# Optimization experiments

Measured on AMD Instinct MI355X. Metric: run time of the kernel, lower is better.

The kernel has to match this reference:

```python
import jax, jax.numpy as jnp
import numpy as np

H, DQS, DQP, DVS, DVP = 12, 16, 4, 16, 8
S_SCALAR = (3.0 * DQS) ** -0.5
S_POINT = (3.0 * DQP * (9.0 * 2.0 ** 0.5)) ** -0.5
S_PAIR = 3.0 ** -0.5
_OFF = np.cumsum([0, H * DQS, H * DQS, H * DVS, H * DQP * 3, H * DQP * 3, H * DVP * 3])


def _ln(x, g, b, eps=1e-5):
    mu = x.mean(-1, keepdims=True)
    var = x.var(-1, keepdims=True)
    return (x - mu) / jnp.sqrt(var + eps) * g + b


def setup_inputs() -> dict:
    B, N, D, PD = 2, 512, 384, 128
    key = jax.random.key(0)
    ks = jax.random.split(key, 12)
    node_feats = jax.random.normal(ks[0], (B, N, D), jnp.float32)
    pair_feats = jax.random.normal(ks[1], (B, N, N, PD), jnp.float32)
    mask = jnp.ones((B, N), dtype=bool)
    # random per-residue rigid frames (orthonormal rotations via QR)
    rot = jnp.linalg.qr(jax.random.normal(ks[2], (B, N, 3, 3), jnp.float32))[0]
    trans = jax.random.normal(ks[3], (B, N, 3), jnp.float32)
    dim_qkv = int(_OFF[-1])             # 1152
    dim_out = H * (PD + DVS + 4 * DVP)  # 2112
    s = 0.02
    p = dict(
        ln_s_g=jnp.ones((D,)), ln_s_b=jnp.zeros((D,)),
        ln_p_g=jnp.ones((PD,)), ln_p_b=jnp.zeros((PD,)),
        w_pair_bias=s * jax.random.normal(ks[4], (PD, H), jnp.float32),
        w_qkv=s * jax.random.normal(ks[5], (D, dim_qkv), jnp.float32),
        point_weights=jnp.full((1, H, 1, 1), float(np.log(np.e - 1.0)), jnp.float32),
        w_out=s * jax.random.normal(ks[6], (dim_out, D), jnp.float32),
        b_out=jnp.zeros((D,)),
        ln_t_g=jnp.ones((D,)), ln_t_b=jnp.zeros((D,)),
        w_ff1=s * jax.random.normal(ks[7], (D, 4 * D), jnp.float32),
        b_ff1=jnp.zeros((4 * D,)),
        w_ff2=s * jax.random.normal(ks[8], (4 * D, D), jnp.float32),
        b_ff2=jnp.zeros((D,)),
    )
    return dict(node_feats=node_feats, pair_feats=pair_feats, mask=mask,
                rot=rot, trans=trans, **p)


def reference(node_feats, pair_feats, mask, rot, trans,
              ln_s_g, ln_s_b, ln_p_g, ln_p_b, w_pair_bias, w_qkv,
              point_weights, w_out, b_out,
              ln_t_g, ln_t_b, w_ff1, b_ff1, w_ff2, b_ff2):
    b, n, d = node_feats.shape
    x = _ln(node_feats, ln_s_g, ln_s_b)
    p = _ln(pair_feats, ln_p_g, ln_p_b)
    pair_bias = jnp.einsum('bijd,dh->bhij', p, w_pair_bias)
    qkv = x @ w_qkv  # (b,n,1152)

    def heads(t, dh):
        return t.reshape(b, n, H, dh).transpose(0, 2, 1, 3)  # b h n d

    q_s = heads(qkv[..., _OFF[0]:_OFF[1]], DQS)
    k_s = heads(qkv[..., _OFF[1]:_OFF[2]], DQS)
    v_s = heads(qkv[..., _OFF[2]:_OFF[3]], DVS)

    def to_pts(t, dp):
        pts = t.reshape(b, n, H * dp, 3)
        # rigid apply: R_i @ x + t_i (global frame)
        pts = jnp.einsum('bnxy,bnpy->bnpx', rot, pts) + trans[:, :, None, :]
        return pts.reshape(b, n, H, dp, 3).transpose(0, 2, 1, 3, 4)  # b h n d 3

    q_p = to_pts(qkv[..., _OFF[3]:_OFF[4]], DQP)
    k_p = to_pts(qkv[..., _OFF[4]:_OFF[5]], DQP)
    v_p = to_pts(qkv[..., _OFF[5]:_OFF[6]], DVP)

    scalar_logits = jnp.einsum('bhid,bhjd->bhij', q_s, k_s)
    # dist attn: -sum_{d,c} (q-k)^2, expanded to avoid (b,h,n,n,d,3) intermediate
    qq = jnp.sum(q_p * q_p, axis=(-1, -2))
    kk = jnp.sum(k_p * k_p, axis=(-1, -2))
    qk = jnp.einsum('bhidc,bhjdc->bhij', q_p, k_p)
    point_logits = -(qq[..., :, None] + kk[..., None, :] - 2.0 * qk)
    point_logits = point_logits * jax.nn.softplus(point_weights)

    neg = jnp.finfo(node_feats.dtype).min
    pm = mask[:, None, :, None] & mask[:, None, None, :]  # b 1 i j
    scalar_logits = jnp.where(pm, scalar_logits, neg)
    point_logits = jnp.where(pm, point_logits, neg)
    pair_bias = jnp.where(pm, pair_bias, neg)

    logits = S_SCALAR * scalar_logits + S_POINT * point_logits + S_PAIR * pair_bias
    attn = jax.nn.softmax(logits, axis=-1)

    out_s = jnp.einsum('bhij,bhjd->bhid', attn, v_s)
    out_pair = jnp.einsum('bhij,bijd->bhid', attn, p)
    out_p = jnp.einsum('bhij,bhjdc->bhidc', attn, v_p)
    # rigid inverse: R_i^T (x - t_i) back to local frame
    pts = out_p.transpose(0, 2, 1, 3, 4).reshape(b, n, H * DVP, 3)
    pts = jnp.einsum('bnyx,bnpy->bnpx', rot, pts - trans[:, :, None, :])
    out_p = pts.reshape(b, n, H, DVP, 3)
    pnorm = jnp.sqrt(jnp.sum(out_p * out_p, axis=-1) + 1e-8)  # safe_norm

    cat = jnp.concatenate([
        out_s.transpose(0, 2, 1, 3).reshape(b, n, H * DVS),
        out_p.reshape(b, n, H * DVP * 3),
        pnorm.reshape(b, n, H * DVP),
        out_pair.transpose(0, 2, 1, 3).reshape(b, n, -1),
    ], axis=-1)
    attn_out = cat @ w_out + b_out

    # residuals + transition (dropout=0 -> identity). Note: transition is
    # applied to attn_out (pre-residual), exactly as in the torch forward.
    node1 = attn_out + node_feats
    t = _ln(attn_out, ln_t_g, ln_t_b)
    t = jax.nn.gelu(t @ w_ff1 + b_ff1) @ w_ff2 + b_ff2
    return t + node1
```

## Files before the change

kernel.cpp:

```cpp
#include <hip/hip_runtime.h>
#include <hip/hip_bf16.h>
#include <math.h>

typedef __hip_bfloat16 bf16;
typedef _Float16 f16;
typedef unsigned short ushort_t;
typedef ushort_t ushort8 __attribute__((ext_vector_type(8)));
typedef ushort_t us4 __attribute__((ext_vector_type(4)));
typedef short bf16x8 __attribute__((ext_vector_type(8)));
typedef f16 f16x8 __attribute__((ext_vector_type(8)));
typedef f16 f16x2 __attribute__((ext_vector_type(2)));
typedef float f32x4 __attribute__((ext_vector_type(4)));
typedef unsigned int u32x4 __attribute__((ext_vector_type(4)));

constexpr float S_SCALAR = 0.14433756729740643f;
constexpr float S_POINT  = 0.08091531528f;
constexpr float S_PAIR   = 0.5773502691896258f;

__device__ inline short f2bfs(float x) {
  return (short)__builtin_bit_cast(unsigned short, __float2bfloat16(x));
}
__device__ inline ushort_t f2bfu(float x) {
  return (ushort_t)__builtin_bit_cast(unsigned short, __float2bfloat16(x));
}
__device__ inline ushort_t f2hu(float x) {
  return __builtin_bit_cast(ushort_t, (f16)x);
}
__device__ inline float h2f(ushort_t u) {
  return (float)__builtin_bit_cast(f16, u);
}
__device__ inline float fdot2f(unsigned a, unsigned b, float c) {
#if __has_builtin(__builtin_amdgcn_fdot2)
  return __builtin_amdgcn_fdot2(__builtin_bit_cast(f16x2, a),
                                __builtin_bit_cast(f16x2, b), c, false);
#else
  f16x2 av = __builtin_bit_cast(f16x2, a), bv = __builtin_bit_cast(f16x2, b);
  return c + (float)av[0] * (float)bv[0] + (float)av[1] * (float)bv[1];
#endif
}

__device__ inline float gelu_tanh(float x) {
  float c = 0.7978845608028654f * (x + 0.044715f * x * x * x);
  return 0.5f * x * (1.f + tanhf(c));
}

__global__ __launch_bounds__(128) void ln384_kernel(
    const float* __restrict__ in, const float* __restrict__ g,
    const float* __restrict__ b, float* __restrict__ out)
{
  int row = blockIdx.x;
  const float* x = in + (size_t)row * 384;
  int t = threadIdx.x;
  float v[3]; float s = 0.f, s2 = 0.f;
#pragma unroll
  for (int i = 0; i < 3; i++) { v[i] = x[t + 128 * i]; s += v[i]; s2 += v[i] * v[i]; }
  for (int o = 32; o; o >>= 1) { s += __shfl_down(s, o); s2 += __shfl_down(s2, o); }
  __shared__ float sh[4];
  int wid = t >> 6, lane = t & 63;
  if (lane == 0) { sh[wid] = s; sh[2 + wid] = s2; }
  __syncthreads();
  s = sh[0] + sh[1]; s2 = sh[2] + sh[3];
  float mean = s * (1.f / 384.f);
  float var = s2 * (1.f / 384.f) - mean * mean;
  float rstd = rsqrtf(fmaxf(var, 0.f) + 1e-5f);
  float* orow = out + (size_t)row * 384;
#pragma unroll
  for (int i = 0; i < 3; i++) {
    int c = t + 128 * i;
    orow[c] = (v[i] - mean) * rstd * g[c] + b[c];
  }
}

__global__ __launch_bounds__(256) void prep_all_kernel(
    const float* __restrict__ w_qkv, const float* __restrict__ w_out,
    const float* __restrict__ w_ff1, const float* __restrict__ w_ff2,
    ushort_t* __restrict__ wqkvT, ushort_t* __restrict__ woutT,
    ushort_t* __restrict__ wff1T, ushort_t* __restrict__ wff2T,
    const float* __restrict__ g, const float* __restrict__ bb,
    const float* __restrict__ wpb, ushort_t* __restrict__ gwbT,
    float* __restrict__ gsbs,
    const float* __restrict__ node, const float* __restrict__ ln_s_g,
    const float* __restrict__ ln_s_b, float* __restrict__ xout)
{
  __shared__ float shmem[2048];
  int bid = blockIdx.x;
  int t = threadIdx.x;
  if (bid < 2376) {
    const float* src; ushort_t* dst; int K, N, bx, by;
    if (bid < 432)       { src = w_qkv; dst = wqkvT; K = 384;  N = 1152; bx = bid % 36;          by = bid / 36; }
    else if (bid < 1224) { src = w_out; dst = woutT; K = 2112; N = 384;  bx = (bid - 432) % 12;  by = (bid - 432) / 12; }
    else if (bid < 1800) { src = w_ff1; dst = wff1T; K = 384;  N = 1536; bx = (bid - 1224) % 48; by = (bid - 1224) / 48; }
    else                 { src = w_ff2; dst = wff2T; K = 1536; N = 384;  bx = (bid - 1800) % 12; by = (bid - 1800) / 12; }
    float (&tile)[32][33] = *reinterpret_cast<float (*)[32][33]>(shmem);
    int n0 = bx * 32, k0 = by * 32;
    int c = t & 31, r4 = (t >> 5) * 4;
#pragma unroll
    for (int i = 0; i < 4; i++)
      tile[r4 + i][c] = src[(size_t)(k0 + r4 + i) * N + n0 + c];
    __syncthreads();
#pragma unroll
    for (int i = 0; i < 4; i++)
      dst[(size_t)(n0 + r4 + i) * K + k0 + c] = f2bfu(tile[c][r4 + i]);
    return;
  }
  if (bid == 2376) {
    for (int idx = t; idx < 2048; idx += 256) {
      int h = idx >> 7, c = idx & 127;
      float v = (h < 12) ? g[c] * wpb[c * 12 + h] : 0.f;
      bf16 r = __float2bfloat16(v);
      gwbT[idx] = __builtin_bit_cast(unsigned short, r);
      shmem[idx] = __bfloat162float(r);
    }
    __syncthreads();
    if (t < 16) {
      float s = 0.f;
      for (int c = 0; c < 128; c++) s += shmem[t * 128 + c];
      gsbs[t] = s;
    } else if (t < 32) {
      int h = t - 16;
      float s = 0.f;
      if (h < 12) for (int c = 0; c < 128; c++) s = fmaf(bb[c], wpb[c * 12 + h], s);
      gsbs[t] = s;
    }
    return;
  }
  int half = t >> 7, tt = t & 127;
  int row = (bid - 2377) * 2 + half;
  const float* x = node + (size_t)row * 384;
  float v[3]; float s = 0.f, s2 = 0.f;
#pragma unroll
  for (int i = 0; i < 3; i++) { v[i] = x[tt + 128 * i]; s += v[i]; s2 += v[i] * v[i]; }
  for (int o = 32; o; o >>= 1) { s += __shfl_down(s, o); s2 += __shfl_down(s2, o); }
  int wid = t >> 6, lane = t & 63;
  if (lane == 0) { shmem[wid] = s; shmem[4 + wid] = s2; }
  __syncthreads();
  s = shmem[half * 2] + shmem[half * 2 + 1];
  s2 = shmem[4 + half * 2] + shmem[4 + half * 2 + 1];
  float mean = s * (1.f / 384.f);
  float var = s2 * (1.f / 384.f) - mean * mean;
  float rstd = rsqrtf(fmaxf(var, 0.f) + 1e-5f);
  float* orow = xout + (size_t)row * 384;
#pragma unroll
  for (int i = 0; i < 3; i++) {
    int c = tt + 128 * i;
    orow[c] = (v[i] - mean) * rstd * ln_s_g[c] + ln_s_b[c];
  }
}

template <int EPI>
__global__ __launch_bounds__(256) void gemm_mfma_kernel(
    const float* __restrict__ A, const ushort_t* __restrict__ BT,
    const float* __restrict__ bias, const float* __restrict__ r1,
    const float* __restrict__ r2, float* __restrict__ C,
    int M, int Nn, int K)
{
  __shared__ ushort_t As[64][72];
  __shared__ ushort_t Bs[64][72];
  int t = threadIdx.x;
  int w = t >> 6, l = t & 63;
  int m0 = blockIdx.y * 64, n0 = blockIdx.x * 64;
  int wm = (w >> 1) * 32, wn = (w & 1) * 32;
  int lr = l & 15, lk = l >> 4;
  int sr = t >> 2, sc = (t & 3) * 16;
  f32x4 acc[2][2];
#pragma unroll
  for (int i = 0; i < 2; i++)
#pragma unroll
    for (int j = 0; j < 2; j++) acc[i][j] = (f32x4){0.f, 0.f, 0.f, 0.f};

  for (int k0 = 0; k0 < K; k0 += 64) {
    const float* Ar = A + (size_t)(m0 + sr) * K + k0 + sc;
    const ushort_t* Br = BT + (size_t)(n0 + sr) * K + k0 + sc;
    float4 a0 = *(const float4*)(Ar + 0);
    float4 a1 = *(const float4*)(Ar + 4);
    float4 a2 = *(const float4*)(Ar + 8);
    float4 a3 = *(const float4*)(Ar + 12);
    ushort8 b0 = *(const ushort8*)(Br + 0);
    ushort8 b1 = *(const ushort8*)(Br + 8);
    ushort8 u0, u1;
    u0[0] = f2bfu(a0.x); u0[1] = f2bfu(a0.y); u0[2] = f2bfu(a0.z); u0[3] = f2bfu(a0.w);
    u0[4] = f2bfu(a1.x); u0[5] = f2bfu(a1.y); u0[6] = f2bfu(a1.z); u0[7] = f2bfu(a1.w);
    u1[0] = f2bfu(a2.x); u1[1] = f2bfu(a2.y); u1[2] = f2bfu(a2.z); u1[3] = f2bfu(a2.w);
    u1[4] = f2bfu(a3.x); u1[5] = f2bfu(a3.y); u1[6] = f2bfu(a3.z); u1[7] = f2bfu(a3.w);
    *(ushort8*)&As[sr][sc] = u0;
    *(ushort8*)&As[sr][sc + 8] = u1;
    *(ushort8*)&Bs[sr][sc] = b0;
    *(ushort8*)&Bs[sr][sc + 8] = b1;
    __syncthreads();
#pragma unroll
    for (int kk = 0; kk < 2; kk++) {
      bf16x8 af0 = *(const bf16x8*)&As[wm + lr][kk * 32 + lk * 8];
      bf16x8 af1 = *(const bf16x8*)&As[wm + 16 + lr][kk * 32 + lk * 8];
      bf16x8 bf0 = *(const bf16x8*)&Bs[wn + lr][kk * 32 + lk * 8];
      bf16x8 bf1 = *(const bf16x8*)&Bs[wn + 16 + lr][kk * 32 + lk * 8];
      acc[0][0] = __builtin_amdgcn_mfma_f32_16x16x32_bf16(af0, bf0, acc[0][0], 0, 0, 0);
      acc[0][1] = __builtin_amdgcn_mfma_f32_16x16x32_bf16(af0, bf1, acc[0][1], 0, 0, 0);
      acc[1][0] = __builtin_amdgcn_mfma_f32_16x16x32_bf16(af1, bf0, acc[1][0], 0, 0, 0);
      acc[1][1] = __builtin_amdgcn_mfma_f32_16x16x32_bf16(af1, bf1, acc[1][1], 0, 0, 0);
    }
    __syncthreads();
  }
#pragma unroll
  for (int mf = 0; mf < 2; mf++) {
#pragma unroll
    for (int nf = 0; nf < 2; nf++) {
      int nn = n0 + wn + nf * 16 + lr;
      float bv = bias ? bias[nn] : 0.f;
#pragma unroll
      for (int e = 0; e < 4; e++) {
        int m = m0 + wm + mf * 16 + lk * 4 + e;
        float v = acc[mf][nf][e] + bv;
        if (EPI == 1) v = gelu_tanh(v);
        if (EPI == 2) v += r1[(size_t)m * Nn + nn] + r2[(size_t)m * Nn + nn];
        C[(size_t)m * Nn + nn] = v;
      }
    }
  }
}

template <int EPI>
__global__ __launch_bounds__(256) void gemm_mfma_m32_kernel(
    const float* __restrict__ A, const ushort_t* __restrict__ BT,
    const float* __restrict__ bias, const float* __restrict__ r1,
    const float* __restrict__ r2, float* __restrict__ C,
    int M, int Nn, int K)
{
  __shared__ ushort_t As[32][72];
  __shared__ ushort_t Bs[64][72];
  int t = threadIdx.x;
  int w = t >> 6, l = t & 63;
  int m0 = blockIdx.y * 32, n0 = blockIdx.x * 64;
  int wm = (w & 1) * 16, wn = (w >> 1) * 32;
  int lr = l & 15, lk = l >> 4;
  int ar = t >> 3, ac = (t & 7) * 8;
  int br = t >> 2, bc = (t & 3) * 16;
  f32x4 acc[2];
  acc[0] = (f32x4){0.f, 0.f, 0.f, 0.f};
  acc[1] = (f32x4){0.f, 0.f, 0.f, 0.f};

  for (int k0 = 0; k0 < K; k0 += 64) {
    const float* Ar = A + (size_t)(m0 + ar) * K + k0 + ac;
    float4 a0 = *(const float4*)(Ar + 0);
    float4 a1 = *(const float4*)(Ar + 4);
    ushort8 u;
    u[0] = f2bfu(a0.x); u[1] = f2bfu(a0.y); u[2] = f2bfu(a0.z); u[3] = f2bfu(a0.w);
    u[4] = f2bfu(a1.x); u[5] = f2bfu(a1.y); u[6] = f2bfu(a1.z); u[7] = f2bfu(a1.w);
    *(ushort8*)&As[ar][ac] = u;
    const ushort_t* Br = BT + (size_t)(n0 + br) * K + k0 + bc;
    *(ushort8*)&Bs[br][bc] = *(const ushort8*)(Br + 0);
    *(ushort8*)&Bs[br][bc + 8] = *(const ushort8*)(Br + 8);
    __syncthreads();
#pragma unroll
    for (int kk = 0; kk < 2; kk++) {
      bf16x8 af = *(const bf16x8*)&As[wm + lr][kk * 32 + lk * 8];
      bf16x8 bf0 = *(const bf16x8*)&Bs[wn + lr][kk * 32 + lk * 8];
      bf16x8 bf1 = *(const bf16x8*)&Bs[wn + 16 + lr][kk * 32 + lk * 8];
      acc[0] = __builtin_amdgcn_mfma_f32_16x16x32_bf16(af, bf0, acc[0], 0, 0, 0);
      acc[1] = __builtin_amdgcn_mfma_f32_16x16x32_bf16(af, bf1, acc[1], 0, 0, 0);
    }
    __syncthreads();
  }
#pragma unroll
  for (int nf = 0; nf < 2; nf++) {
    int nn = n0 + wn + nf * 16 + lr;
    float bv = bias ? bias[nn] : 0.f;
#pragma unroll
    for (int e = 0; e < 4; e++) {
      int m = m0 + wm + lk * 4 + e;
      float v = acc[nf][e] + bv;
      if (EPI == 1) v = gelu_tanh(v);
      if (EPI == 2) v += r1[(size_t)m * Nn + nn] + r2[(size_t)m * Nn + nn];
      C[(size_t)m * Nn + nn] = v;
    }
  }
}

__global__ __launch_bounds__(256) void qkv_post_kernel(
    const float* __restrict__ qkv, const float* __restrict__ rot,
    const float* __restrict__ trans, const float* __restrict__ pw,
    f16* __restrict__ qhat, f16* __restrict__ khat,
    ushort_t* __restrict__ vT)
{
  int bh = blockIdx.x;
  int b = bh / 12, h = bh - b * 12;
  int role = blockIdx.y >> 1;
  int j = (blockIdx.y & 1) * 256 + threadIdx.x;
  int bn = b * 512 + j;
  const float* row = qkv + (size_t)bn * 1152;
  float R[9];
#pragma unroll
  for (int k = 0; k < 9; k++) R[k] = rot[bn * 9 + k];
  float T0 = trans[bn * 3], T1 = trans[bn * 3 + 1], T2 = trans[bn * 3 + 2];
  if (role == 0) {
    float sp = log1pf(__expf(pw[h]));
    float c1 = 2.f * S_POINT * sp;
    float spp = S_POINT * sp;
    f16* qh = qhat + ((size_t)bh * 512 + j) * 32;
#pragma unroll
    for (int d = 0; d < 16; d++) qh[d] = (f16)(S_SCALAR * row[h * 16 + d]);
#pragma unroll
    for (int p = 0; p < 4; p++) {
      int base = 576 + (h * 4 + p) * 3;
      float x = row[base], y = row[base + 1], z = row[base + 2];
      qh[16 + p * 3 + 0] = (f16)(c1 * (R[0] * x + R[1] * y + R[2] * z + T0));
      qh[16 + p * 3 + 1] = (f16)(c1 * (R[3] * x + R[4] * y + R[5] * z + T1));
      qh[16 + p * 3 + 2] = (f16)(c1 * (R[6] * x + R[7] * y + R[8] * z + T2));
    }
    qh[28] = (f16)(-spp);
    qh[29] = (f16)0.f; qh[30] = (f16)0.f; qh[31] = (f16)0.f;
  } else if (role == 1) {
    f16* kh = khat + ((size_t)bh * 512 + j) * 32;
#pragma unroll
    for (int d = 0; d < 16; d++) kh[d] = (f16)(row[192 + h * 16 + d]);
    float kksum = 0.f;
#pragma unroll
    for (int p = 0; p < 4; p++) {
      int base = 720 + (h * 4 + p) * 3;
      float x = row[base], y = row[base + 1], z = row[base + 2];
      float gx = R[0] * x + R[1] * y + R[2] * z + T0;
      float gy = R[3] * x + R[4] * y + R[5] * z + T1;
      float gz = R[6] * x + R[7] * y + R[8] * z + T2;
      kh[16 + p * 3 + 0] = (f16)gx; kh[16 + p * 3 + 1] = (f16)gy; kh[16 + p * 3 + 2] = (f16)gz;
      kksum = fmaf(gx, gx, kksum); kksum = fmaf(gy, gy, kksum); kksum = fmaf(gz, gz, kksum);
    }
    kh[28] = (f16)kksum;
    kh[29] = (f16)0.f; kh[30] = (f16)0.f; kh[31] = (f16)0.f;
  } else {
    ushort_t* vt = vT + (size_t)bh * 40 * 512;
#pragma unroll
    for (int c = 0; c < 16; c++) vt[c * 512 + j] = f2hu(row[384 + h * 16 + c]);
#pragma unroll
    for (int p = 0; p < 8; p++) {
      int base = 864 + (h * 8 + p) * 3;
      float x = row[base], y = row[base + 1], z = row[base + 2];
      vt[(16 + p * 3 + 0) * 512 + j] = f2hu(R[0] * x + R[1] * y + R[2] * z + T0);
      vt[(16 + p * 3 + 1) * 512 + j] = f2hu(R[3] * x + R[4] * y + R[5] * z + T1);
      vt[(16 + p * 3 + 2) * 512 + j] = f2hu(R[6] * x + R[7] * y + R[8] * z + T2);
    }
  }
}

__global__ __launch_bounds__(256) void mega_kernel(
    const float* __restrict__ pair, const ushort_t* __restrict__ gwbT,
    const float* __restrict__ gsbs, const float* __restrict__ g,
    const float* __restrict__ bb, const f16* __restrict__ qhat,
    const f16* __restrict__ khat, ushort_t* __restrict__ attnb,
    float* __restrict__ cat)
{
  __shared__ ushort_t tile[128][136];
  __shared__ ushort_t Ps[16][520];
  __shared__ ushort_t bias_s[16][136];
  __shared__ unsigned qhat_u[12][16];
  __shared__ float red_s[2][6][4];
  __shared__ float m_s[16], l_s[16], r_s[16], invl_s[16];
  __shared__ float mhist_s[4][16], cf_s[4][16];

  int bn = blockIdx.x;
  int b = bn >> 9, i = bn & 511;
  int t = threadIdx.x;
  int wv = t >> 6, ln = t & 63, lr = ln & 15, lk = ln >> 4;

  if (t < 16) { m_s[t] = -3.0e38f; l_s[t] = 0.f; r_s[t] = 1.f; }
  for (int idx = t; idx < 4 * 520; idx += 256) Ps[12 + idx / 520][idx % 520] = 0;
  if (t < 192) {
    int h = t >> 4, d4 = t & 15;
    qhat_u[h][d4] = ((const unsigned*)qhat)[((size_t)(b * 12 + h) * 512 + i) * 16 + d4];
  }
  bf16x8 bfrag[4];
#pragma unroll
  for (int kc = 0; kc < 4; kc++) {
    const ushort_t* gp = gwbT + lr * 128 + kc * 32 + lk * 8;
    us4 q0 = *(const us4*)gp;
    us4 q1 = *(const us4*)(gp + 4);
    bfrag[kc][0] = (short)q0[0]; bfrag[kc][1] = (short)q0[1];
    bfrag[kc][2] = (short)q0[2]; bfrag[kc][3] = (short)q0[3];
    bfrag[kc][4] = (short)q1[0]; bfrag[kc][5] = (short)q1[1];
    bfrag[kc][6] = (short)q1[2]; bfrag[kc][7] = (short)q1[3];
  }
  float gsum = gsbs[lr];
  float bsP = S_PAIR * gsbs[16 + lr];
  int n0 = wv * 32;
  int sw0 = (((n0 + lr) >> 3) & 7) << 4;
  int sw1 = (((n0 + 16 + lr) >> 3) & 7) << 4;
  f32x4 po0 = {0.f, 0.f, 0.f, 0.f}, po1 = {0.f, 0.f, 0.f, 0.f};
  __syncthreads();

  for (int ck = 0; ck < 4; ck++) {
    int jc = ck * 128;
    const float* p0 = pair + ((size_t)bn * 512 + jc + wv * 32 + lr) * 128 + lk * 8;
    f32x4 acc0 = {0.f, 0.f, 0.f, 0.f}, acc1 = {0.f, 0.f, 0.f, 0.f};
    float s0 = 0.f, s20 = 0.f, s1 = 0.f, s21 = 0.f;
#pragma unroll
    for (int kc = 0; kc < 4; kc++) {
      float4 u0 = *(const float4*)(p0 + kc * 32);
      float4 u1 = *(const float4*)(p0 + kc * 32 + 4);
      float4 w0 = *(const float4*)(p0 + 2048 + kc * 32);
      float4 w1 = *(const float4*)(p0 + 2048 + kc * 32 + 4);
      s0 += u0.x + u0.y + u0.z + u0.w + u1.x + u1.y + u1.z + u1.w;
      s20 = fmaf(u0.x, u0.x, s20); s20 = fmaf(u0.y, u0.y, s20);
      s20 = fmaf(u0.z, u0.z, s20); s20 = fmaf(u0.w, u0.w, s20);
      s20 = fmaf(u1.x, u1.x, s20); s20 = fmaf(u1.y, u1.y, s20);
      s20 = fmaf(u1.z, u1.z, s20); s20 = fmaf(u1.w, u1.w, s20);
      s1 += w0.x + w0.y + w0.z + w0.w + w1.x + w1.y + w1.z + w1.w;
      s21 = fmaf(w0.x, w0.x, s21); s21 = fmaf(w0.y, w0.y, s21);
      s21 = fmaf(w0.z, w0.z, s21); s21 = fmaf(w0.w, w0.w, s21);
      s21 = fmaf(w1.x, w1.x, s21); s21 = fmaf(w1.y, w1.y, s21);
      s21 = fmaf(w1.z, w1.z, s21); s21 = fmaf(w1.w, w1.w, s21);
      bf16x8 a0, a1;
      a0[0] = f2bfs(u0.x); a0[1] = f2bfs(u0.y); a0[2] = f2bfs(u0.z); a0[3] = f2bfs(u0.w);
      a0[4] = f2bfs(u1.x); a0[5] = f2bfs(u1.y); a0[6] = f2bfs(u1.z); a0[7] = f2bfs(u1.w);
      a1[0] = f2bfs(w0.x); a1[1] = f2bfs(w0.y); a1[2] = f2bfs(w0.z); a1[3] = f2bfs(w0.w);
      a1[4] = f2bfs(w1.x); a1[5] = f2bfs(w1.y); a1[6] = f2bfs(w1.z); a1[7] = f2bfs(w1.w);
      acc0 = __builtin_amdgcn_mfma_f32_16x16x32_bf16(a0, bfrag[kc], acc0, 0, 0, 0);
      acc1 = __builtin_amdgcn_mfma_f32_16x16x32_bf16(a1, bfrag[kc], acc1, 0, 0, 0);
    }
    s0 += __shfl_xor(s0, 16);  s0 += __shfl_xor(s0, 32);
    s20 += __shfl_xor(s20, 16); s20 += __shfl_xor(s20, 32);
    s1 += __shfl_xor(s1, 16);  s1 += __shfl_xor(s1, 32);
    s21 += __shfl_xor(s21, 16); s21 += __shfl_xor(s21, 32);
    float mean0 = s0 * (1.f / 128.f);
    float rstd0 = rsqrtf(fmaxf(s20 * (1.f / 128.f) - mean0 * mean0, 0.f) + 1e-5f);
    float mean1 = s1 * (1.f / 128.f);
    float rstd1 = rsqrtf(fmaxf(s21 * (1.f / 128.f) - mean1 * mean1, 0.f) + 1e-5f);
    int jl_u = wv * 32 + lr, jl_w = wv * 32 + 16 + lr;
#pragma unroll
    for (int kc = 0; kc < 4; kc++) {
      int c0 = kc * 32 + lk * 8;
      float4 u0 = *(const float4*)(p0 + kc * 32);
      float4 u1 = *(const float4*)(p0 + kc * 32 + 4);
      float4 w0 = *(const float4*)(p0 + 2048 + kc * 32);
      float4 w1 = *(const float4*)(p0 + 2048 + kc * 32 + 4);
      float4 g0 = *(const float4*)(g + c0);
      float4 g1 = *(const float4*)(g + c0 + 4);
      float4 b0 = *(const float4*)(bb + c0);
      float4 b1 = *(const float4*)(bb + c0 + 4);
      float uu[8] = {u0.x, u0.y, u0.z, u0.w, u1.x, u1.y, u1.z, u1.w};
      float ww[8] = {w0.x, w0.y, w0.z, w0.w, w1.x, w1.y, w1.z, w1.w};
      float gg[8] = {g0.x, g0.y, g0.z, g0.w, g1.x, g1.y, g1.z, g1.w};
      float bv[8] = {b0.x, b0.y, b0.z, b0.w, b1.x, b1.y, b1.z, b1.w};
#pragma unroll
      for (int e = 0; e < 8; e++) {
        int c = c0 + e;
        int sw = ((c >> 3) & 7) << 4;
        tile[c][jl_u ^ sw] = f2hu(fmaf((uu[e] - mean0) * rstd0, gg[e], bv[e]));
        tile[c][jl_w ^ sw] = f2hu(fmaf((ww[e] - mean1) * rstd1, gg[e], bv[e]));
      }
    }
    {
      us4 pk0, pk1;
#pragma unroll
      for (int e = 0; e < 4; e++) {
        int r = lk * 4 + e;
        float m0 = __shfl(mean0, r), rs0 = __shfl(rstd0, r);
        float m1 = __shfl(mean1, r), rs1 = __shfl(rstd1, r);
        pk0[e] = f2hu(fmaf(S_PAIR * rs0, acc0[e] - m0 * gsum, bsP));
        pk1[e] = f2hu(fmaf(S_PAIR * rs1, acc1[e] - m1 * gsum, bsP));
      }
      *(us4*)&bias_s[lr][wv * 32 + lk * 4] = pk0;
      *(us4*)&bias_s[lr][wv * 32 + 16 + lk * 4] = pk1;
    }
    __syncthreads();
    float lgv[6];
#pragma unroll
    for (int q = 0; q < 6; q++) {
      int h = 2 * q + (wv >> 1);
      int jl = (wv & 1) * 64 + ln;
      const u32x4* kr = (const u32x4*)(khat + ((size_t)(b * 12 + h) * 512 + jc + jl) * 32);
      float d = 0.f;
#pragma unroll
      for (int qq = 0; qq < 4; qq++) {
        u32x4 kv = kr[qq];
        u32x4 qv = *(const u32x4*)&qhat_u[h][qq * 4];
        d = fdot2f(kv[0], qv[0], d);
        d = fdot2f(kv[1], qv[1], d);
        d = fdot2f(kv[2], qv[2], d);
        d = fdot2f(kv[3], qv[3], d);
      }
      lgv[q] = d + h2f(bias_s[h][jl]);
    }
#pragma unroll
    for (int q = 0; q < 6; q++) {
      float m = lgv[q];
      m = fmaxf(m, __shfl_xor(m, 1));  m = fmaxf(m, __shfl_xor(m, 2));
      m = fmaxf(m, __shfl_xor(m, 4));  m = fmaxf(m, __shfl_xor(m, 8));
      m = fmaxf(m, __shfl_xor(m, 16)); m = fmaxf(m, __shfl_xor(m, 32));
      if (ln == 0) red_s[0][q][wv] = m;
    }
    __syncthreads();
    if (t < 12) {
      int q = t >> 1, wp = (t & 1) * 2;
      float cm = fmaxf(red_s[0][q][wp], red_s[0][q][wp + 1]);
      float mo = m_s[t];
      float mn = fmaxf(mo, cm);
      m_s[t] = mn; r_s[t] = __expf(mo - mn); mhist_s[ck][t] = mn;
    }
    __syncthreads();
#pragma unroll
    for (int q = 0; q < 6; q++) {
      int h = 2 * q + (wv >> 1);
      int jl = (wv & 1) * 64 + ln;
      float p = __expf(lgv[q] - m_s[h]);
      Ps[h][jc + jl] = f2hu(p);
      float s = p;
      s += __shfl_xor(s, 1);  s += __shfl_xor(s, 2);
      s += __shfl_xor(s, 4);  s += __shfl_xor(s, 8);
      s += __shfl_xor(s, 16); s += __shfl_xor(s, 32);
      if (ln == 0) red_s[1][q][wv] = s;
    }
#pragma unroll
    for (int e = 0; e < 4; e++) {
      float rr = r_s[lk * 4 + e];
      po0[e] *= rr; po1[e] *= rr;
    }
    __syncthreads();
    if (t < 12) {
      int q = t >> 1, wp = (t & 1) * 2;
      l_s[t] = l_s[t] * r_s[t] + red_s[1][q][wp] + red_s[1][q][wp + 1];
    }
#pragma unroll
    for (int ks = 0; ks < 4; ks++) {
      int kb = ks * 32 + lk * 8;
      f16x8 af = *(const f16x8*)&Ps[lr][jc + kb];
      f16x8 b0 = *(const f16x8*)&tile[n0 + lr][kb ^ sw0];
      f16x8 b1 = *(const f16x8*)&tile[n0 + 16 + lr][kb ^ sw1];
      po0 = __builtin_amdgcn_mfma_f32_16x16x32_f16(af, b0, po0, 0, 0, 0);
      po1 = __builtin_amdgcn_mfma_f32_16x16x32_f16(af, b1, po1, 0, 0, 0);
    }
    __syncthreads();
  }
  if (t < 64) {
    int c = t >> 4, h = t & 15;
    cf_s[c][h] = __expf(mhist_s[c][h] - m_s[h]);
  }
  if (t < 16) invl_s[t] = 1.f / l_s[t];
  __syncthreads();
  ushort_t* arow = attnb + (size_t)bn * 12 * 512;
#pragma unroll
  for (int it = 0; it < 24; it++) {
    int idx = t + 256 * it;
    int h = idx >> 9, j = idx & 511;
    float v = h2f(Ps[h][j]) * cf_s[j >> 7][h] * invl_s[h];
    arow[(size_t)h * 512 + j] = f2hu(v);
  }
  float* crow = cat + (size_t)bn * 2112 + 576;
#pragma unroll
  for (int e = 0; e < 4; e++) {
    int hh = lk * 4 + e;
    if (hh < 12) {
      float il = invl_s[hh];
      crow[hh * 128 + n0 + lr] = po0[e] * il;
      crow[hh * 128 + n0 + 16 + lr] = po1[e] * il;
    }
  }
}

__global__ __launch_bounds__(256) void sv_gemm_kernel(
    const ushort_t* __restrict__ attn, const ushort_t* __restrict__ vT,
    float* __restrict__ svraw)
{
  int i0 = blockIdx.x * 64;
  int bh = blockIdx.y;
  int b = bh / 12, h = bh - b * 12;
  __shared__ ushort_t As_[64][72];
  __shared__ ushort_t Bs_[48][72];
  int t = threadIdx.x;
  int w = t >> 6, l = t & 63, lr = l & 15, lk = l >> 4;
  int ai = t >> 2, as = (t & 3) * 16;
  const ushort_t* vbase = vT + (size_t)bh * 40 * 512;
  f32x4 acc[3];
#pragma unroll
  for (int n = 0; n < 3; n++) acc[n] = (f32x4){0.f, 0.f, 0.f, 0.f};

  for (int jt = 0; jt < 8; jt++) {
    int jb = jt * 64;
    size_t aoff = ((size_t)(b * 512 + i0 + ai) * 12 + h) * 512 + jb + as;
    ushort8 a0 = *(const ushort8*)(attn + aoff);
    ushort8 a1 = *(const ushort8*)(attn + aoff + 8);
    *(ushort8*)&As_[ai][as] = a0;
    *(ushort8*)&As_[ai][as + 8] = a1;
    for (int idx = t; idx < 384; idx += 256) {
      int c = idx >> 3, j8 = (idx & 7) * 8;
      ushort8 v = {0, 0, 0, 0, 0, 0, 0, 0};
      if (c < 40) v = *(const ushort8*)(vbase + (size_t)c * 512 + jb + j8);
      *(ushort8*)&Bs_[c][j8] = v;
    }
    __syncthreads();
#pragma unroll
    for (int kk = 0; kk < 2; kk++) {
      f16x8 af = *(const f16x8*)&As_[w * 16 + lr][kk * 32 + lk * 8];
#pragma unroll
      for (int n = 0; n < 3; n++) {
        f16x8 bf_ = *(const f16x8*)&Bs_[n * 16 + lr][kk * 32 + lk * 8];
        acc[n] = __builtin_amdgcn_mfma_f32_16x16x32_f16(af, bf_, acc[n], 0, 0, 0);
      }
    }
    __syncthreads();
  }
#pragma unroll
  for (int n = 0; n < 3; n++) {
    int c = n * 16 + lr;
    if (c < 40) {
#pragma unroll
      for (int e = 0; e < 4; e++) {
        int i = i0 + w * 16 + lk * 4 + e;
        svraw[(size_t)(b * 512 + i) * 480 + h * 40 + c] = acc[n][e];
      }
    }
  }
}

__global__ __launch_bounds__(192) void sv_epilogue_kernel(
    const float* __restrict__ svraw, const float* __restrict__ rot,
    const float* __restrict__ trans, float* __restrict__ cat)
{
  int bn = blockIdx.x;
  const float* sv = svraw + (size_t)bn * 480;
  float* crow = cat + (size_t)bn * 2112;
  int t = threadIdx.x;
  {
    int h2 = t >> 4, d = t & 15;
    crow[t] = sv[h2 * 40 + d];
  }
  if (t < 96) {
    int h2 = t >> 3, dp = t & 7;
    float T0 = trans[bn * 3], T1 = trans[bn * 3 + 1], T2 = trans[bn * 3 + 2];
    const float* R = rot + bn * 9;
    float px = sv[h2 * 40 + 16 + dp * 3 + 0] - T0;
    float py = sv[h2 * 40 + 16 + dp * 3 + 1] - T1;
    float pz = sv[h2 * 40 + 16 + dp * 3 + 2] - T2;
    float lx = R[0] * px + R[3] * py + R[6] * pz;
    float ly = R[1] * px + R[4] * py + R[7] * pz;
    float lz = R[2] * px + R[5] * py + R[8] * pz;
    crow[192 + h2 * 24 + dp * 3 + 0] = lx;
    crow[192 + h2 * 24 + dp * 3 + 1] = ly;
    crow[192 + h2 * 24 + dp * 3 + 2] = lz;
    crow[480 + h2 * 8 + dp] = sqrtf(lx * lx + ly * ly + lz * lz + 1e-8f);
  }
}

extern "C" void kernel_launch(void* const* d_in, const int* in_sizes, int n_in,
                              void* d_out, int out_size, void* d_ws, size_t ws_size,
                              hipStream_t stream)
{
  const float* node   = (const float*)d_in[0];
  const float* pair   = (const float*)d_in[1];
  const float* rot    = (const float*)d_in[3];
  const float* trans  = (const float*)d_in[4];
  const float* ln_s_g = (const float*)d_in[5];
  const float* ln_s_b = (const float*)d_in[6];
  const float* ln_p_g = (const float*)d_in[7];
  const float* ln_p_b = (const float*)d_in[8];
  const float* wpb    = (const float*)d_in[9];
  const float* w_qkv  = (const float*)d_in[10];
  const float* pw     = (const float*)d_in[11];
  const float* w_out  = (const float*)d_in[12];
  const float* b_out  = (const float*)d_in[13];
  const float* ln_t_g = (const float*)d_in[14];
  const float* ln_t_b = (const float*)d_in[15];
  const float* w_ff1  = (const float*)d_in[16];
  const float* b_ff1  = (const float*)d_in[17];
  const float* w_ff2  = (const float*)d_in[18];
  const float* b_ff2  = (const float*)d_in[19];
  float* out = (float*)d_out;
  float* ws = (float*)d_ws;

  float* qkv    = ws;
  float* x      = ws + 1179648;
  float* tn     = x;
  float* ao     = ws + 1572864;
  float* svraw  = ws + 1966080;
  float* cat    = ws + 2457600;
  ushort_t* attnb = (ushort_t*)(ws + 5603328);
  float* gb     = ws + 5603328;
  ushort_t* gwbT = (ushort_t*)(ws + 8749056);
  float* gsbs   = ws + 8750080;
  ushort_t* wqkvT = (ushort_t*)(ws + 8750112);
  ushort_t* woutT = (ushort_t*)(ws + 8971296);
  ushort_t* wff1T = (ushort_t*)(ws + 9376800);
  ushort_t* wff2T = (ushort_t*)(ws + 9671712);
  f16* qhat     = (f16*)(ws + 9966624);
  f16* khat     = (f16*)(ws + 10163232);
  ushort_t* vT  = (ushort_t*)(ws + 10359840);

  prep_all_kernel<<<2889, 256, 0, stream>>>(w_qkv, w_out, w_ff1, w_ff2,
      wqkvT, woutT, wff1T, wff2T, ln_p_g, ln_p_b, wpb, gwbT, gsbs,
      node, ln_s_g, ln_s_b, x);
  gemm_mfma_kernel<0><<<dim3(18, 16), 256, 0, stream>>>(x, wqkvT, nullptr, nullptr, nullptr, qkv, 1024, 1152, 384);
  qkv_post_kernel<<<dim3(24, 6), 256, 0, stream>>>(qkv, rot, trans, pw, qhat, khat, vT);
  mega_kernel<<<1024, 256, 0, stream>>>(pair, gwbT, gsbs, ln_p_g, ln_p_b, qhat, khat, attnb, cat);
  sv_gemm_kernel<<<dim3(8, 24), 256, 0, stream>>>(attnb, vT, svraw);
  sv_epilogue_kernel<<<1024, 192, 0, stream>>>(svraw, rot, trans, cat);
  gemm_mfma_m32_kernel<0><<<dim3(6, 32), 256, 0, stream>>>(cat, woutT, b_out, nullptr, nullptr, ao, 1024, 384, 2112);
  ln384_kernel<<<1024, 128, 0, stream>>>(ao, ln_t_g, ln_t_b, tn);
  gemm_mfma_kernel<1><<<dim3(24, 16), 256, 0, stream>>>(tn, wff1T, b_ff1, nullptr, nullptr, gb, 1024, 1536, 384);
  gemm_mfma_m32_kernel<2><<<dim3(6, 32), 256, 0, stream>>>(gb, wff2T, b_ff2, ao, node, out, 1024, 384, 1536);
}
```

Before: 606.3 us.

## Double-buffer pair loads, restructure softmax per-warp-per-head, repack khat layout

Pair-feature chunks are now prefetched into registers one chunk ahead (double buffering), so global loads overlap the LayerNorm/bias compute. The softmax is reorganised so each warp owns whole heads, with max and sum reduced inside the warp instead of across warps through shared memory. This drops two __syncthreads per chunk. khat is repacked into an 8-element-group planar layout so adjacent lanes read adjacent 16-byte vectors. Padded head rows and shared arrays shrink to 12, and launch_bounds asks for 2 blocks per CU, which risks register pressure from the two 16-float4 buffers.

```diff
diff --git a/kernel.cpp b/kernel.cpp
--- a/kernel.cpp
+++ b/kernel.cpp
@@ -278,7 +278,7 @@
 __global__ __launch_bounds__(256) void qkv_post_kernel(
     const float* __restrict__ qkv, const float* __restrict__ rot,
     const float* __restrict__ trans, const float* __restrict__ pw,
-    f16* __restrict__ qhat, f16* __restrict__ khat,
+    f16* __restrict__ qhat, ushort_t* __restrict__ khatP,
     ushort_t* __restrict__ vT)
 {
   int bh = blockIdx.x;
@@ -309,9 +309,9 @@
     qh[28] = (f16)(-spp);
     qh[29] = (f16)0.f; qh[30] = (f16)0.f; qh[31] = (f16)0.f;
   } else if (role == 1) {
-    f16* kh = khat + ((size_t)bh * 512 + j) * 32;
-#pragma unroll
-    for (int d = 0; d < 16; d++) kh[d] = (f16)(row[192 + h * 16 + d]);
+    float kv[32];
+#pragma unroll
+    for (int d = 0; d < 16; d++) kv[d] = row[192 + h * 16 + d];
     float kksum = 0.f;
 #pragma unroll
     for (int p = 0; p < 4; p++) {
@@ -320,11 +320,18 @@
       float gx = R[0] * x + R[1] * y + R[2] * z + T0;
       float gy = R[3] * x + R[4] * y + R[5] * z + T1;
       float gz = R[6] * x + R[7] * y + R[8] * z + T2;
-      kh[16 + p * 3 + 0] = (f16)gx; kh[16 + p * 3 + 1] = (f16)gy; kh[16 + p * 3 + 2] = (f16)gz;
+      kv[16 + p * 3 + 0] = gx; kv[16 + p * 3 + 1] = gy; kv[16 + p * 3 + 2] = gz;
       kksum = fmaf(gx, gx, kksum); kksum = fmaf(gy, gy, kksum); kksum = fmaf(gz, gz, kksum);
     }
-    kh[28] = (f16)kksum;
-    kh[29] = (f16)0.f; kh[30] = (f16)0.f; kh[31] = (f16)0.f;
+    kv[28] = kksum; kv[29] = 0.f; kv[30] = 0.f; kv[31] = 0.f;
+    ushort_t* kp = khatP + ((size_t)bh * 4) * 512 * 8 + (size_t)j * 8;
+#pragma unroll
+    for (int dg = 0; dg < 4; dg++) {
+      ushort8 u;
+#pragma unroll
+      for (int e = 0; e < 8; e++) u[e] = f2hu(kv[dg * 8 + e]);
+      *(ushort8*)(kp + (size_t)dg * 512 * 8) = u;
+    }
   } else {
     ushort_t* vt = vT + (size_t)bh * 40 * 512;
 #pragma unroll
@@ -340,28 +347,27 @@
   }
 }
 
-__global__ __launch_bounds__(256) void mega_kernel(
+__global__ __launch_bounds__(256, 2) void mega_kernel(
     const float* __restrict__ pair, const ushort_t* __restrict__ gwbT,
     const float* __restrict__ gsbs, const float* __restrict__ g,
     const float* __restrict__ bb, const f16* __restrict__ qhat,
-    const f16* __restrict__ khat, ushort_t* __restrict__ attnb,
+    const ushort_t* __restrict__ khatP, ushort_t* __restrict__ attnb,
     float* __restrict__ cat)
 {
   __shared__ ushort_t tile[128][136];
-  __shared__ ushort_t Ps[16][520];
-  __shared__ ushort_t bias_s[16][136];
+  __shared__ ushort_t Ps[12][520];
+  __shared__ ushort_t bias_s[12][136];
   __shared__ unsigned qhat_u[12][16];
-  __shared__ float red_s[2][6][4];
-  __shared__ float m_s[16], l_s[16], r_s[16], invl_s[16];
-  __shared__ float mhist_s[4][16], cf_s[4][16];
+  __shared__ float m_s[12], l_s[12], r_s[16], invl_s[12];
+  __shared__ float mhist_s[4][12], cf_s[4][12];
 
   int bn = blockIdx.x;
   int b = bn >> 9, i = bn & 511;
   int t = threadIdx.x;
   int wv = t >> 6, ln = t & 63, lr = ln & 15, lk = ln >> 4;
 
-  if (t < 16) { m_s[t] = -3.0e38f; l_s[t] = 0.f; r_s[t] = 1.f; }
-  for (int idx = t; idx < 4 * 520; idx += 256) Ps[12 + idx / 520][idx % 520] = 0;
+  if (t < 12) { m_s[t] = -3.0e38f; l_s[t] = 0.f; }
+  if (t < 16) r_s[t] = 1.f;
   if (t < 192) {
     int h = t >> 4, d4 = t & 15;
     qhat_u[h][d4] = ((const unsigned*)qhat)[((size_t)(b * 12 + h) * 512 + i) * 16 + d4];
@@ -383,19 +389,23 @@
   int sw0 = (((n0 + lr) >> 3) & 7) << 4;
   int sw1 = (((n0 + 16 + lr) >> 3) & 7) << 4;
   f32x4 po0 = {0.f, 0.f, 0.f, 0.f}, po1 = {0.f, 0.f, 0.f, 0.f};
-  __syncthreads();
-
-  for (int ck = 0; ck < 4; ck++) {
-    int jc = ck * 128;
-    const float* p0 = pair + ((size_t)bn * 512 + jc + wv * 32 + lr) * 128 + lk * 8;
+
+  const float* pbase = pair + ((size_t)bn * 512 + wv * 32 + lr) * 128 + lk * 8;
+
+#define LOADP(buf, ckk) do { const float* pp_ = pbase + (size_t)(ckk) * 16384; \
+  _Pragma("unroll") for (int kc_ = 0; kc_ < 4; kc_++) { \
+    buf[kc_ * 4 + 0] = *(const float4*)(pp_ + kc_ * 32); \
+    buf[kc_ * 4 + 1] = *(const float4*)(pp_ + kc_ * 32 + 4); \
+    buf[kc_ * 4 + 2] = *(const float4*)(pp_ + 2048 + kc_ * 32); \
+    buf[kc_ * 4 + 3] = *(const float4*)(pp_ + 2048 + kc_ * 32 + 4); } } while (0)
+
+  auto phaseA = [&](const float4 (&pv)[16]) {
     f32x4 acc0 = {0.f, 0.f, 0.f, 0.f}, acc1 = {0.f, 0.f, 0.f, 0.f};
     float s0 = 0.f, s20 = 0.f, s1 = 0.f, s21 = 0.f;
 #pragma unroll
     for (int kc = 0; kc < 4; kc++) {
-      float4 u0 = *(const float4*)(p0 + kc * 32);
-      float4 u1 = *(const float4*)(p0 + kc * 32 + 4);
-      float4 w0 = *(const float4*)(p0 + 2048 + kc * 32);
-      float4 w1 = *(const float4*)(p0 + 2048 + kc * 32 + 4);
+      float4 u0 = pv[kc * 4 + 0], u1 = pv[kc * 4 + 1];
+      float4 w0 = pv[kc * 4 + 2], w1 = pv[kc * 4 + 3];
       s0 += u0.x + u0.y + u0.z + u0.w + u1.x + u1.y + u1.z + u1.w;
       s20 = fmaf(u0.x, u0.x, s20); s20 = fmaf(u0.y, u0.y, s20);
       s20 = fmaf(u0.z, u0.z, s20); s20 = fmaf(u0.w, u0.w, s20);
@@ -426,10 +436,8 @@
 #pragma unroll
     for (int kc = 0; kc < 4; kc++) {
       int c0 = kc * 32 + lk * 8;
-      float4 u0 = *(const float4*)(p0 + kc * 32);
-      float4 u1 = *(const float4*)(p0 + kc * 32 + 4);
-      float4 w0 = *(const float4*)(p0 + 2048 + kc * 32);
-      float4 w1 = *(const float4*)(p0 + 2048 + kc * 32 + 4);
+      float4 u0 = pv[kc * 4 + 0], u1 = pv[kc * 4 + 1];
+      float4 w0 = pv[kc * 4 + 2], w1 = pv[kc * 4 + 3];
       float4 g0 = *(const float4*)(g + c0);
       float4 g1 = *(const float4*)(g + c0 + 4);
       float4 b0 = *(const float4*)(bb + c0);
@@ -446,81 +454,81 @@
         tile[c][jl_w ^ sw] = f2hu(fmaf((ww[e] - mean1) * rstd1, gg[e], bv[e]));
       }
     }
-    {
-      us4 pk0, pk1;
-#pragma unroll
-      for (int e = 0; e < 4; e++) {
-        int r = lk * 4 + e;
-        float m0 = __shfl(mean0, r), rs0 = __shfl(rstd0, r);
-        float m1 = __shfl(mean1, r), rs1 = __shfl(rstd1, r);
-        pk0[e] = f2hu(fmaf(S_PAIR * rs0, acc0[e] - m0 * gsum, bsP));
-        pk1[e] = f2hu(fmaf(S_PAIR * rs1, acc1[e] - m1 * gsum, bsP));
-      }
+    us4 pk0, pk1;
+#pragma unroll
+    for (int e = 0; e < 4; e++) {
+      int r = lk * 4 + e;
+      float m0 = __shfl(mean0, r), rs0 = __shfl(rstd0, r);
+      float m1 = __shfl(mean1, r), rs1 = __shfl(rstd1, r);
+      pk0[e] = f2hu(fmaf(S_PAIR * rs0, acc0[e] - m0 * gsum, bsP));
+      pk1[e] = f2hu(fmaf(S_PAIR * rs1, acc1[e] - m1 * gsum, bsP));
+    }
+    if (lr < 12) {
       *(us4*)&bias_s[lr][wv * 32 + lk * 4] = pk0;
       *(us4*)&bias_s[lr][wv * 32 + 16 + lk * 4] = pk1;
     }
-    __syncthreads();
-    float lgv[6];
-#pragma unroll
-    for (int q = 0; q < 6; q++) {
-      int h = 2 * q + (wv >> 1);
-      int jl = (wv & 1) * 64 + ln;
-      const u32x4* kr = (const u32x4*)(khat + ((size_t)(b * 12 + h) * 512 + jc + jl) * 32);
-      float d = 0.f;
-#pragma unroll
-      for (int qq = 0; qq < 4; qq++) {
-        u32x4 kv = kr[qq];
-        u32x4 qv = *(const u32x4*)&qhat_u[h][qq * 4];
-        d = fdot2f(kv[0], qv[0], d);
-        d = fdot2f(kv[1], qv[1], d);
-        d = fdot2f(kv[2], qv[2], d);
-        d = fdot2f(kv[3], qv[3], d);
+  };
+
+  float4 bufA[16], bufB[16];
+  LOADP(bufA, 0);
+  __syncthreads();
+
+  for (int ck = 0; ck < 4; ck++) {
+    int jc = ck * 128;
+    if ((ck & 1) == 0) {
+      if (ck < 3) LOADP(bufB, ck + 1);
+      phaseA(bufA);
+    } else {
+      if (ck < 3) LOADP(bufA, ck + 1);
+      phaseA(bufB);
+    }
+    __syncthreads();
+#pragma unroll
+    for (int q = 0; q < 3; q++) {
+      int h = wv + q * 4;
+      const u32x4* kp = (const u32x4*)khatP + (size_t)(b * 12 + h) * 4 * 512;
+      float d0 = 0.f, d1 = 0.f;
+#pragma unroll
+      for (int dg = 0; dg < 4; dg++) {
+        u32x4 qv = *(const u32x4*)&qhat_u[h][dg * 4];
+        u32x4 k0 = kp[dg * 512 + jc + ln];
+        u32x4 k1 = kp[dg * 512 + jc + 64 + ln];
+        d0 = fdot2f(k0[0], qv[0], d0); d0 = fdot2f(k0[1], qv[1], d0);
+        d0 = fdot2f(k0[2], qv[2], d0); d0 = fdot2f(k0[3], qv[3], d0);
+        d1 = fdot2f(k1[0], qv[0], d1); d1 = fdot2f(k1[1], qv[1], d1);
+        d1 = fdot2f(k1[2], qv[2], d1); d1 = fdot2f(k1[3], qv[3], d1);
       }
-      lgv[q] = d + h2f(bias_s[h][jl]);
-    }
-#pragma unroll
-    for (int q = 0; q < 6; q++) {
-      float m = lgv[q];
-      m = fmaxf(m, __shfl_xor(m, 1));  m = fmaxf(m, __shfl_xor(m, 2));
-      m = fmaxf(m, __shfl_xor(m, 4));  m = fmaxf(m, __shfl_xor(m, 8));
-      m = fmaxf(m, __shfl_xor(m, 16)); m = fmaxf(m, __shfl_xor(m, 32));
-      if (ln == 0) red_s[0][q][wv] = m;
-    }
-    __syncthreads();
-    if (t < 12) {
-      int q = t >> 1, wp = (t & 1) * 2;
-      float cm = fmaxf(red_s[0][q][wp], red_s[0][q][wp + 1]);
-      float mo = m_s[t];
-      float mn = fmaxf(mo, cm);
-      m_s[t] = mn; r_s[t] = __expf(mo - mn); mhist_s[ck][t] = mn;
-    }
-    __syncthreads();
-#pragma unroll
-    for (int q = 0; q < 6; q++) {
-      int h = 2 * q + (wv >> 1);
-      int jl = (wv & 1) * 64 + ln;
-      float p = __expf(lgv[q] - m_s[h]);
-      Ps[h][jc + jl] = f2hu(p);
-      float s = p;
+      d0 += h2f(bias_s[h][ln]);
+      d1 += h2f(bias_s[h][64 + ln]);
+      float lm = fmaxf(d0, d1);
+      lm = fmaxf(lm, __shfl_xor(lm, 1));  lm = fmaxf(lm, __shfl_xor(lm, 2));
+      lm = fmaxf(lm, __shfl_xor(lm, 4));  lm = fmaxf(lm, __shfl_xor(lm, 8));
+      lm = fmaxf(lm, __shfl_xor(lm, 16)); lm = fmaxf(lm, __shfl_xor(lm, 32));
+      float mo = m_s[h];
+      float mn = fmaxf(mo, lm);
+      float r = __expf(mo - mn);
+      float p0 = __expf(d0 - mn), p1 = __expf(d1 - mn);
+      Ps[h][jc + ln] = f2hu(p0);
+      Ps[h][jc + 64 + ln] = f2hu(p1);
+      float s = p0 + p1;
       s += __shfl_xor(s, 1);  s += __shfl_xor(s, 2);
       s += __shfl_xor(s, 4);  s += __shfl_xor(s, 8);
       s += __shfl_xor(s, 16); s += __shfl_xor(s, 32);
-      if (ln == 0) red_s[1][q][wv] = s;
-    }
+      if (ln == 0) {
+        m_s[h] = mn; l_s[h] = l_s[h] * r + s; r_s[h] = r; mhist_s[ck][h] = mn;
+      }
+    }
+    __syncthreads();
 #pragma unroll
     for (int e = 0; e < 4; e++) {
       float rr = r_s[lk * 4 + e];
       po0[e] *= rr; po1[e] *= rr;
     }
-    __syncthreads();
-    if (t < 12) {
-      int q = t >> 1, wp = (t & 1) * 2;
-      l_s[t] = l_s[t] * r_s[t] + red_s[1][q][wp] + red_s[1][q][wp + 1];
-    }
+    int arow_c = (lr < 12) ? lr : 11;
 #pragma unroll
     for (int ks = 0; ks < 4; ks++) {
       int kb = ks * 32 + lk * 8;
-      f16x8 af = *(const f16x8*)&Ps[lr][jc + kb];
+      f16x8 af = *(const f16x8*)&Ps[arow_c][jc + kb];
       f16x8 b0 = *(const f16x8*)&tile[n0 + lr][kb ^ sw0];
       f16x8 b1 = *(const f16x8*)&tile[n0 + 16 + lr][kb ^ sw1];
       po0 = __builtin_amdgcn_mfma_f32_16x16x32_f16(af, b0, po0, 0, 0, 0);
@@ -528,11 +536,12 @@
     }
     __syncthreads();
   }
-  if (t < 64) {
-    int c = t >> 4, h = t & 15;
+#undef LOADP
+  if (t < 48) {
+    int c = t / 12, h = t - c * 12;
     cf_s[c][h] = __expf(mhist_s[c][h] - m_s[h]);
   }
-  if (t < 16) invl_s[t] = 1.f / l_s[t];
+  if (t < 12) invl_s[t] = 1.f / l_s[t];
   __syncthreads();
   ushort_t* arow = attnb + (size_t)bn * 12 * 512;
 #pragma unroll
@@ -679,15 +688,15 @@
   ushort_t* wff1T = (ushort_t*)(ws + 9376800);
   ushort_t* wff2T = (ushort_t*)(ws + 9671712);
   f16* qhat     = (f16*)(ws + 9966624);
-  f16* khat     = (f16*)(ws + 10163232);
+  ushort_t* khatP = (ushort_t*)(ws + 10163232);
   ushort_t* vT  = (ushort_t*)(ws + 10359840);
 
   prep_all_kernel<<<2889, 256, 0, stream>>>(w_qkv, w_out, w_ff1, w_ff2,
       wqkvT, woutT, wff1T, wff2T, ln_p_g, ln_p_b, wpb, gwbT, gsbs,
       node, ln_s_g, ln_s_b, x);
   gemm_mfma_kernel<0><<<dim3(18, 16), 256, 0, stream>>>(x, wqkvT, nullptr, nullptr, nullptr, qkv, 1024, 1152, 384);
-  qkv_post_kernel<<<dim3(24, 6), 256, 0, stream>>>(qkv, rot, trans, pw, qhat, khat, vT);
-  mega_kernel<<<1024, 256, 0, stream>>>(pair, gwbT, gsbs, ln_p_g, ln_p_b, qhat, khat, attnb, cat);
+  qkv_post_kernel<<<dim3(24, 6), 256, 0, stream>>>(qkv, rot, trans, pw, qhat, khatP, vT);
+  mega_kernel<<<1024, 256, 0, stream>>>(pair, gwbT, gsbs, ln_p_g, ln_p_b, qhat, khatP, attnb, cat);
   sv_gemm_kernel<<<dim3(8, 24), 256, 0, stream>>>(attnb, vT, svraw);
   sv_epilogue_kernel<<<1024, 192, 0, stream>>>(svraw, rot, trans, cat);
   gemm_mfma_m32_kernel<0><<<dim3(6, 32), 256, 0, stream>>>(cat, woutT, b_out, nullptr, nullptr, ao, 1024, 384, 2112);
```

New measurement: 578.8 us. -4.5%, faster.
